# Kernel tuning notes

Hardware: AMD Instinct MI355X
Metric: run time of the kernel (lower is better)

The kernel has to match this reference:

```python
import jax, jax.numpy as jnp
import numpy as np

B, NF, IN = 8, 4096, 512
NB, NW, CD = 2, 320, 384  # num_codebooks, num_codewords, codeword_dim (d_model=NB*CD=768)
TAU = 1.0


def setup_inputs() -> dict:
    key = jax.random.key(0)
    k0, k1, k2, k3, k4 = jax.random.split(key, 5)
    x = jax.random.normal(k0, (B, NF, IN), dtype=jnp.float32)
    mask = jax.random.randint(k1, (B, NF), 0, 2) == 1  # True = invalid frame
    u = jax.random.uniform(k2, (B, NF, NB, NW), jnp.float32, 1e-6, 1.0 - 1e-6)
    gumbel = -jnp.log(-jnp.log(u))
    # projection Linear(IN -> NB*NW)
    W = jax.random.normal(k3, (IN, NB * NW), jnp.float32) * np.float32(1.0 / np.sqrt(IN))
    b = jnp.zeros((NB * NW,), jnp.float32)
    # codebooks, xavier-uniform-ish init
    limit = np.float32(np.sqrt(6.0 / (NW + CD)))
    codebooks = jax.random.uniform(k4, (NB, NW, CD), jnp.float32, -limit, limit)
    return dict(x=x, W=W, b=b, codebooks=codebooks, gumbel=gumbel, mask=mask)


def reference(x, W, b, codebooks, gumbel, mask):
    Bx, NFx = x.shape[:2]
    logits = (x @ W + b).reshape(Bx, NFx, NB, NW)  # (b, nf, nb, nw)
    # hard gumbel-softmax with straight-through estimator (training path)
    y = (logits + gumbel) / TAU
    soft = jax.nn.softmax(y, axis=-1)
    hard = jax.nn.one_hot(jnp.argmax(y, axis=-1), NW, dtype=soft.dtype)
    word_probs = hard + soft - jax.lax.stop_gradient(soft)
    # diversity perplexity from plain softmax probs, masked; note: faithful to
    # source, normalization divides by mask.sum() (count of invalid frames)
    soft_probs = jax.nn.softmax(logits, axis=-1)
    valid = (~mask)[..., None, None].astype(soft_probs.dtype)
    marginal = jnp.sum(soft_probs * valid, axis=(0, 1)) / mask.sum().astype(soft_probs.dtype)
    perplexity = jnp.exp(-jnp.sum(marginal * jnp.log(marginal + 1e-7), axis=-1)).sum()
    # quantize: one-hot gather-sum over codewords, concat codebooks -> d_model
    quantized = jnp.einsum('bfnw,nwd->bfnd', word_probs, codebooks).reshape(Bx, NFx, NB * CD)
    return quantized, perplexity
```

## Files before the change

kernel.cpp:

```cpp
#include <hip/hip_runtime.h>
#include <math.h>

#define BQ   8
#define NFQ  4096
#define INQ  512
#define NBQ  2
#define NWQ  320
#define CDQ  384
#define MQ   (BQ*NFQ)
#define NTOT (NBQ*NWQ)
#define DMOD (NBQ*CDQ)
#define QOUT ((size_t)MQ*(size_t)DMOD)

#define THREADS 512
#define BM 64
#define BK 32
#define NCH (INQ/BK)
#define NMB (MQ/BM)

#define A0B 0
#define A1B 4096
#define B0B 8192
#define B1B 28672
#define SMEMB 49152
#define SSUMB 8192
#define AYMB  9216
#define AIDXB 10240
#define SCB   11264
#define IDXB  11520
#define CALB  11776

#define WT_OFF   0
#define PART_OFF 655360
#define CS_OFF   1310720
#define MC_OFF   1313280

typedef __attribute__((ext_vector_type(4))) float f32x4;
typedef __attribute__((ext_vector_type(8))) short short8;
typedef const __attribute__((address_space(1))) unsigned short gas_us;
typedef __attribute__((address_space(3))) unsigned short las_us;

static __device__ __forceinline__ unsigned f2bf(float f) {
    unsigned u = __float_as_uint(f);
    return (u + 0x7FFFu + ((u >> 16) & 1u)) >> 16;
}

static __device__ __forceinline__ uint4 pack8u(float4 a, float4 b) {
    return make_uint4(f2bf(a.x) | (f2bf(a.y) << 16),
                      f2bf(a.z) | (f2bf(a.w) << 16),
                      f2bf(b.x) | (f2bf(b.y) << 16),
                      f2bf(b.z) | (f2bf(b.w) << 16));
}

#define MCOL(M,N) \
  acc##M##N = __builtin_amdgcn_mfma_f32_16x16x32_bf16(fa##M, fb##N, acc##M##N,0,0,0);

#define STAGE_B(KC, BASE) do { \
  const unsigned short* wp_ = WtB + (KC)*BK; \
  __builtin_amdgcn_global_load_lds((gas_us*)(wp_ + gb0), (las_us*)(smem + (BASE) + lo0), 16, 0, 0); \
  __builtin_amdgcn_global_load_lds((gas_us*)(wp_ + gb1), (las_us*)(smem + (BASE) + lo1), 16, 0, 0); \
  if (tid < 256) \
    __builtin_amdgcn_global_load_lds((gas_us*)(wp_ + gb2), (las_us*)(smem + (BASE) + lo2), 16, 0, 0); \
} while(0)

#define EPI1(M,R) do { \
  const int row_ = rh*32 + M*16 + q*4 + (R); \
  const int gm_  = m0 + row_; \
  float s_ = __expf(acc##M##0[R]) + __expf(acc##M##1[R]) + __expf(acc##M##2[R]) \
           + __expf(acc##M##3[R]) + __expf(acc##M##4[R]); \
  s_ += __shfl_xor(s_,1,64); s_ += __shfl_xor(s_,2,64); \
  s_ += __shfl_xor(s_,4,64); s_ += __shfl_xor(s_,8,64); \
  const float* gp_ = gum + (size_t)gm_*NTOT + nb*NWQ + cg*80 + c15; \
  float ym_ = acc##M##0[R] + gp_[0]; int yi_ = c15; float yt_; \
  yt_ = acc##M##1[R] + gp_[16]; if (yt_>ym_){ym_=yt_; yi_=16+c15;} \
  yt_ = acc##M##2[R] + gp_[32]; if (yt_>ym_){ym_=yt_; yi_=32+c15;} \
  yt_ = acc##M##3[R] + gp_[48]; if (yt_>ym_){ym_=yt_; yi_=48+c15;} \
  yt_ = acc##M##4[R] + gp_[64]; if (yt_>ym_){ym_=yt_; yi_=64+c15;} \
  yi_ += cg*80; \
  { float ov_; int oi_; \
    ov_=__shfl_xor(ym_,1,64); oi_=__shfl_xor(yi_,1,64); if(ov_>ym_||(ov_==ym_&&oi_<yi_)){ym_=ov_;yi_=oi_;} \
    ov_=__shfl_xor(ym_,2,64); oi_=__shfl_xor(yi_,2,64); if(ov_>ym_||(ov_==ym_&&oi_<yi_)){ym_=ov_;yi_=oi_;} \
    ov_=__shfl_xor(ym_,4,64); oi_=__shfl_xor(yi_,4,64); if(ov_>ym_||(ov_==ym_&&oi_<yi_)){ym_=ov_;yi_=oi_;} \
    ov_=__shfl_xor(ym_,8,64); oi_=__shfl_xor(yi_,8,64); if(ov_>ym_||(ov_==ym_&&oi_<yi_)){ym_=ov_;yi_=oi_;} } \
  if (c15 == 0) { \
    ((float*)(smem+SSUMB))[cg*64 + row_] = s_; \
    ((float*)(smem+AYMB ))[cg*64 + row_] = ym_; \
    ((int*  )(smem+AIDXB))[cg*64 + row_] = yi_; } \
} while(0)

#define EPI2(M,R) do { \
  const int row_ = rh*32 + M*16 + q*4 + (R); \
  const float sc_ = ((float*)(smem+SCB))[row_]; \
  ca0 = fmaf(__expf(acc##M##0[R]), sc_, ca0); \
  ca1 = fmaf(__expf(acc##M##1[R]), sc_, ca1); \
  ca2 = fmaf(__expf(acc##M##2[R]), sc_, ca2); \
  ca3 = fmaf(__expf(acc##M##3[R]), sc_, ca3); \
  ca4 = fmaf(__expf(acc##M##4[R]), sc_, ca4); \
} while(0)

__global__ __launch_bounds__(256) void wcvt(const float* __restrict__ W,
                                            unsigned short* __restrict__ Wt)
{
    __shared__ __align__(16) float sm[64][68];
    const int kb = blockIdx.x, cbk = blockIdx.y;
    const int tid = threadIdx.x;
    const int r = tid >> 2, qq = tid & 3;
    const float* wp = W + (size_t)(kb*64 + r)*NTOT + cbk*64;
    *(float4*)(&sm[r][(qq   )*4]) = *(const float4*)(wp + (qq   )*4);
    *(float4*)(&sm[r][(qq+ 4)*4]) = *(const float4*)(wp + (qq+ 4)*4);
    *(float4*)(&sm[r][(qq+ 8)*4]) = *(const float4*)(wp + (qq+ 8)*4);
    *(float4*)(&sm[r][(qq+12)*4]) = *(const float4*)(wp + (qq+12)*4);
    __syncthreads();
    const int cc = tid >> 2, kq = tid & 3;
    const int k0 = kq * 16;
    const float v0=sm[k0+0][cc],  v1=sm[k0+1][cc],  v2=sm[k0+2][cc],  v3=sm[k0+3][cc],
                v4=sm[k0+4][cc],  v5=sm[k0+5][cc],  v6=sm[k0+6][cc],  v7=sm[k0+7][cc],
                v8=sm[k0+8][cc],  v9=sm[k0+9][cc],  v10=sm[k0+10][cc],v11=sm[k0+11][cc],
                v12=sm[k0+12][cc],v13=sm[k0+13][cc],v14=sm[k0+14][cc],v15=sm[k0+15][cc];
    const unsigned u0 = f2bf(v0)  | (f2bf(v1) <<16), u1 = f2bf(v2)  | (f2bf(v3) <<16),
                   u2 = f2bf(v4)  | (f2bf(v5) <<16), u3 = f2bf(v6)  | (f2bf(v7) <<16),
                   u4 = f2bf(v8)  | (f2bf(v9) <<16), u5 = f2bf(v10) | (f2bf(v11)<<16),
                   u6 = f2bf(v12) | (f2bf(v13)<<16), u7 = f2bf(v14) | (f2bf(v15)<<16);
    unsigned short* op = Wt + (size_t)(cbk*64 + cc)*INQ + kb*64 + k0;
    *(uint4*)(op)     = make_uint4(u0,u1,u2,u3);
    *(uint4*)(op + 8) = make_uint4(u4,u5,u6,u7);
}

__global__ __launch_bounds__(THREADS, 4) void qk1(
    const float* __restrict__ x, const unsigned short* __restrict__ Wt,
    const float* __restrict__ bias, const float* __restrict__ cb,
    const float* __restrict__ gum, const int* __restrict__ maskp,
    float* __restrict__ out, unsigned short* __restrict__ partial)
{
    __shared__ __align__(16) char smem[SMEMB];
    const int tid = threadIdx.x;
    const int bid = blockIdx.x;
    const int mb = bid >> 1, nb = bid & 1;
    const int m0 = mb * BM;
    const int w = tid >> 6, l = tid & 63, q = l >> 4, c15 = l & 15;
    const int cg = w & 3, rh = w >> 2;

    const int sB = tid & 3;
    const int colj0 = (tid      ) >> 2, colj1 = (tid +  512) >> 2,
              colj2 = (tid + 1024) >> 2;
    const int kgj0 = sB ^ ((colj0 >> 1) & 3), kgj1 = sB ^ ((colj1 >> 1) & 3),
              kgj2 = sB ^ ((colj2 >> 1) & 3);
    const unsigned short* WtB = Wt + (size_t)nb * NWQ * INQ;
    const int gb0 = colj0*INQ + kgj0*8, gb1 = colj1*INQ + kgj1*8,
              gb2 = colj2*INQ + kgj2*8;
    const int lo0 = (tid      )*16, lo1 = (tid+ 512)*16, lo2 = (tid+1024)*16;

    const int xrow = tid >> 2, xh = tid & 3;
    const float* xg = x + (size_t)(m0 + xrow)*INQ + xh*8;
    const int axw = xrow*64 + ((xh ^ ((xrow >> 1) & 3)) * 16);

    const int sw = (c15 >> 1) & 3;
    const int aoff = (rh*32 + c15)*64 + ((q ^ sw) * 16);
    const int boff = (cg*80 + c15)*64 + ((q ^ sw) * 16);

    f32x4 acc00={0,0,0,0}, acc01={0,0,0,0}, acc02={0,0,0,0}, acc03={0,0,0,0}, acc04={0,0,0,0};
    f32x4 acc10={0,0,0,0}, acc11={0,0,0,0}, acc12={0,0,0,0}, acc13={0,0,0,0}, acc14={0,0,0,0};

    STAGE_B(0, B0B);
    if (tid < 256) {
        const float4 a0 = *(const float4*)(xg), a1 = *(const float4*)(xg + 4);
        *(uint4*)(smem + A0B + axw) = pack8u(a0, a1);
    }
    __syncthreads();

#pragma unroll 2
    for (int kc = 0; kc < NCH; ++kc) {
        const int p = kc & 1;
        const int Acur = p ? A1B : A0B;
        const int Anx  = p ? A0B : A1B;
        const int Bcur = p ? B1B : B0B;
        const int Bnx  = p ? B0B : B1B;
        const bool more = (kc + 1 < NCH);
        float4 n0, n1;
        if (more) {
            if (tid < 256) {
                n0 = *(const float4*)(xg + (kc+1)*BK);
                n1 = *(const float4*)(xg + (kc+1)*BK + 4);
            }
            STAGE_B(kc + 1, Bnx);
        }
        const short8 fa0 = *(const short8*)(smem + Acur + aoff);
        const short8 fa1 = *(const short8*)(smem + Acur + aoff + 1024);
        const short8 fb0 = *(const short8*)(smem + Bcur + boff);
        const short8 fb1 = *(const short8*)(smem + Bcur + boff + 1024);
        const short8 fb2 = *(const short8*)(smem + Bcur + boff + 2048);
        const short8 fb3 = *(const short8*)(smem + Bcur + boff + 3072);
        const short8 fb4 = *(const short8*)(smem + Bcur + boff + 4096);
        MCOL(0,0); MCOL(0,1); MCOL(0,2); MCOL(0,3); MCOL(0,4);
        MCOL(1,0); MCOL(1,1); MCOL(1,2); MCOL(1,3); MCOL(1,4);
        if (more && tid < 256)
            *(uint4*)(smem + Anx + axw) = pack8u(n0, n1);
        __syncthreads();
    }

    const float* bp = bias + nb*NWQ + cg*80 + c15;
    const float b0v = bp[0], b1v = bp[16], b2v = bp[32], b3v = bp[48], b4v = bp[64];
    acc00 = acc00 + b0v; acc01 = acc01 + b1v; acc02 = acc02 + b2v;
    acc03 = acc03 + b3v; acc04 = acc04 + b4v;
    acc10 = acc10 + b0v; acc11 = acc11 + b1v; acc12 = acc12 + b2v;
    acc13 = acc13 + b3v; acc14 = acc14 + b4v;

    EPI1(0,0); EPI1(0,1); EPI1(0,2); EPI1(0,3);
    EPI1(1,0); EPI1(1,1); EPI1(1,2); EPI1(1,3);
    __syncthreads();

    if (tid < BM) {
        const int row = tid;
        const float* ssum = (const float*)(smem + SSUMB);
        const float* aym  = (const float*)(smem + AYMB);
        const int*   aidx = (const int*)(smem + AIDXB);
        const float se = ssum[row] + ssum[64+row] + ssum[128+row] + ssum[192+row];
        const float vf = (maskp[m0 + row] == 0) ? 1.0f : 0.0f;
        ((float*)(smem + SCB))[row] = vf / se;
        float bv = aym[row]; int bi = aidx[row];
        float ov; int oi;
        ov = aym[ 64+row]; oi = aidx[ 64+row]; if (ov>bv || (ov==bv && oi<bi)) { bv=ov; bi=oi; }
        ov = aym[128+row]; oi = aidx[128+row]; if (ov>bv || (ov==bv && oi<bi)) { bv=ov; bi=oi; }
        ov = aym[192+row]; oi = aidx[192+row]; if (ov>bv || (ov==bv && oi<bi)) { bv=ov; bi=oi; }
        ((int*)(smem + IDXB))[row] = bi;
    }
    __syncthreads();

    float ca0=0.f, ca1=0.f, ca2=0.f, ca3=0.f, ca4=0.f;
    EPI2(0,0); EPI2(0,1); EPI2(0,2); EPI2(0,3);
    EPI2(1,0); EPI2(1,1); EPI2(1,2); EPI2(1,3);
    ca0 += __shfl_xor(ca0,16,64); ca0 += __shfl_xor(ca0,32,64);
    ca1 += __shfl_xor(ca1,16,64); ca1 += __shfl_xor(ca1,32,64);
    ca2 += __shfl_xor(ca2,16,64); ca2 += __shfl_xor(ca2,32,64);
    ca3 += __shfl_xor(ca3,16,64); ca3 += __shfl_xor(ca3,32,64);
    ca4 += __shfl_xor(ca4,16,64); ca4 += __shfl_xor(ca4,32,64);
    if (l < 16) {
        float* cal = (float*)(smem + CALB) + w*80 + c15;
        cal[0]=ca0; cal[16]=ca1; cal[32]=ca2; cal[48]=ca3; cal[64]=ca4;
    }
    __syncthreads();
    if (tid < NWQ) {
        const float* cal = (const float*)(smem + CALB);
        const float v = cal[tid] + cal[tid + 320];
        partial[(size_t)mb*NTOT + nb*NWQ + tid] = (unsigned short)f2bf(v);
    }

    const float* cbb = cb + (size_t)nb*NWQ*CDQ;
    const int* idxs = (const int*)(smem + IDXB);
    for (int t = tid; t < BM*(CDQ/4); t += THREADS) {
        const int r = t / (CDQ/4);
        const int qq = t - r*(CDQ/4);
        const int idx = idxs[r];
        float4 v = *(const float4*)(cbb + (size_t)idx*CDQ + qq*4);
        *(float4*)(out + (size_t)(m0+r)*DMOD + (size_t)nb*CDQ + qq*4) = v;
    }
}

__global__ __launch_bounds__(256) void qk2a(const unsigned short* __restrict__ partial,
                                            const int* __restrict__ maskp,
                                            float* __restrict__ colsum,
                                            int* __restrict__ maskcnt)
{
    __shared__ float fs[256];
    __shared__ int   is[4];
    const int b = blockIdx.x, tid = threadIdx.x;
    if (b < 40) {
        const int ci = tid & 15, g = tid >> 4;
        const int col = b*16 + ci;
        float s = 0.f;
        for (int r = 0; r < 32; ++r) {
            const unsigned u = partial[(size_t)(g*32 + r)*NTOT + col];
            s += __uint_as_float(u << 16);
        }
        fs[g*16 + ci] = s;
        __syncthreads();
        if (tid < 16) {
            float t = 0.f;
            for (int g2 = 0; g2 < 16; ++g2) t += fs[g2*16 + tid];
            colsum[b*16 + tid] = t;
        }
    } else {
        const int bb = b - 40;
        int ms = 0;
        for (int k2 = 0; k2 < 16; ++k2) ms += maskp[bb*4096 + tid + k2*256];
        for (int s2 = 32; s2 >= 1; s2 >>= 1) ms += __shfl_xor(ms, s2, 64);
        if ((tid & 63) == 0) is[tid >> 6] = ms;
        __syncthreads();
        if (tid == 0) maskcnt[bb] = is[0] + is[1] + is[2] + is[3];
    }
}

__global__ void qk2b(const float* __restrict__ colsum,
                     const int* __restrict__ maskcnt,
                     float* __restrict__ out)
{
    __shared__ float fred[10];
    __shared__ float s_ms;
    const int tid = threadIdx.x, lane = tid & 63, wid = tid >> 6;
    if (tid == 0) {
        int t = 0;
        for (int i = 0; i < 8; ++i) t += maskcnt[i];
        s_ms = (float)t;
    }
    __syncthreads();
    float mar = colsum[tid] / s_ms;
    float tv = mar * logf(mar + 1e-7f);
    for (int s = 32; s >= 1; s >>= 1) tv += __shfl_xor(tv, s, 64);
    if (lane == 0) fred[wid] = tv;
    __syncthreads();
    if (tid == 0) {
        float h0 = fred[0]+fred[1]+fred[2]+fred[3]+fred[4];
        float h1 = fred[5]+fred[6]+fred[7]+fred[8]+fred[9];
        out[QOUT] = expf(-h0) + expf(-h1);
    }
}

extern "C" void kernel_launch(void* const* d_in, const int* in_sizes, int n_in,
                              void* d_out, int out_size, void* d_ws, size_t ws_size,
                              hipStream_t stream) {
    const float* x    = (const float*)d_in[0];
    const float* W    = (const float*)d_in[1];
    const float* bias = (const float*)d_in[2];
    const float* cb   = (const float*)d_in[3];
    const float* gum  = (const float*)d_in[4];
    const int*   mask = (const int*)d_in[5];
    float* out = (float*)d_out;
    unsigned short* Wt      = (unsigned short*)((char*)d_ws + WT_OFF);
    unsigned short* partial = (unsigned short*)((char*)d_ws + PART_OFF);
    float*          colsum  = (float*)((char*)d_ws + CS_OFF);
    int*            maskcnt = (int*)((char*)d_ws + MC_OFF);

    wcvt<<<dim3(INQ/64, NTOT/64), 256, 0, stream>>>(W, Wt);
    qk1<<<NMB*NBQ, THREADS, 0, stream>>>(x, Wt, bias, cb, gum, mask, out, partial);
    qk2a<<<48, 256, 0, stream>>>(partial, mask, colsum, maskcnt);
    qk2b<<<1, 640, 0, stream>>>(colsum, maskcnt, out);
}
```

Before: 77.81 us.

## Warp-specialize GEMM main loop: B-loaders and A-converters with deeper x prefetch

Splits the 8 waves into two roles: waves 0-3 issue all the direct-to-LDS weight loads (five per thread instead of three spread across the block), and waves 4-7 load the fp32 x tile, convert it to bf16 and write it to LDS. The x register prefetch now runs two chunks ahead, and the main loop is manually unrolled with explicit waitcnt plus s_barrier instead of __syncthreads. The goal is to hide global load latency behind the MFMAs and to remove divergent per-thread guards. In exchange the work per wave is unbalanced and the explicit waitcnt(0) forces the loader waves to stall on their loads before each barrier.

```diff
diff --git a/kernel.cpp b/kernel.cpp
--- a/kernel.cpp
+++ b/kernel.cpp
@@ -59,8 +59,29 @@
   const unsigned short* wp_ = WtB + (KC)*BK; \
   __builtin_amdgcn_global_load_lds((gas_us*)(wp_ + gb0), (las_us*)(smem + (BASE) + lo0), 16, 0, 0); \
   __builtin_amdgcn_global_load_lds((gas_us*)(wp_ + gb1), (las_us*)(smem + (BASE) + lo1), 16, 0, 0); \
-  if (tid < 256) \
-    __builtin_amdgcn_global_load_lds((gas_us*)(wp_ + gb2), (las_us*)(smem + (BASE) + lo2), 16, 0, 0); \
+  __builtin_amdgcn_global_load_lds((gas_us*)(wp_ + gb2), (las_us*)(smem + (BASE) + lo2), 16, 0, 0); \
+  __builtin_amdgcn_global_load_lds((gas_us*)(wp_ + gb3), (las_us*)(smem + (BASE) + lo3), 16, 0, 0); \
+  __builtin_amdgcn_global_load_lds((gas_us*)(wp_ + gb4), (las_us*)(smem + (BASE) + lo4), 16, 0, 0); \
+} while(0)
+
+#define KBODY(KC, CUR0, CUR1, NXT0, NXT1, ACUR, ANXT, BCUR, BNXT) do { \
+  if (isB) { STAGE_B((KC)+1, BNXT); } \
+  else { NXT0 = *(const float4*)(xg + ((KC)+2)*BK); \
+         NXT1 = *(const float4*)(xg + ((KC)+2)*BK + 4); } \
+  const short8 fa0 = *(const short8*)(smem + (ACUR) + aoff); \
+  const short8 fa1 = *(const short8*)(smem + (ACUR) + aoff + 1024); \
+  const short8 fb0 = *(const short8*)(smem + (BCUR) + boff); \
+  const short8 fb1 = *(const short8*)(smem + (BCUR) + boff + 1024); \
+  const short8 fb2 = *(const short8*)(smem + (BCUR) + boff + 2048); \
+  const short8 fb3 = *(const short8*)(smem + (BCUR) + boff + 3072); \
+  const short8 fb4 = *(const short8*)(smem + (BCUR) + boff + 4096); \
+  MCOL(0,0); MCOL(0,1); MCOL(0,2); MCOL(0,3); MCOL(0,4); \
+  MCOL(1,0); MCOL(1,1); MCOL(1,2); MCOL(1,3); MCOL(1,4); \
+  if (isB) { asm volatile("s_waitcnt vmcnt(0)" ::: "memory"); } \
+  else     { *(uint4*)(smem + (ANXT) + axw) = pack8u(CUR0, CUR1); } \
+  asm volatile("s_waitcnt lgkmcnt(0)" ::: "memory"); \
+  __builtin_amdgcn_s_barrier(); \
+  asm volatile("" ::: "memory"); \
 } while(0)
 
 #define EPI1(M,R) do { \
@@ -139,18 +160,24 @@
     const int m0 = mb * BM;
     const int w = tid >> 6, l = tid & 63, q = l >> 4, c15 = l & 15;
     const int cg = w & 3, rh = w >> 2;
+    const bool isB = (w < 4);
 
     const int sB = tid & 3;
-    const int colj0 = (tid      ) >> 2, colj1 = (tid +  512) >> 2,
-              colj2 = (tid + 1024) >> 2;
+    const int colj0 = (tid      ) >> 2, colj1 = (tid +  256) >> 2,
+              colj2 = (tid + 512) >> 2, colj3 = (tid +  768) >> 2,
+              colj4 = (tid +1024) >> 2;
     const int kgj0 = sB ^ ((colj0 >> 1) & 3), kgj1 = sB ^ ((colj1 >> 1) & 3),
-              kgj2 = sB ^ ((colj2 >> 1) & 3);
+              kgj2 = sB ^ ((colj2 >> 1) & 3), kgj3 = sB ^ ((colj3 >> 1) & 3),
+              kgj4 = sB ^ ((colj4 >> 1) & 3);
     const unsigned short* WtB = Wt + (size_t)nb * NWQ * INQ;
     const int gb0 = colj0*INQ + kgj0*8, gb1 = colj1*INQ + kgj1*8,
-              gb2 = colj2*INQ + kgj2*8;
-    const int lo0 = (tid      )*16, lo1 = (tid+ 512)*16, lo2 = (tid+1024)*16;
-
-    const int xrow = tid >> 2, xh = tid & 3;
+              gb2 = colj2*INQ + kgj2*8, gb3 = colj3*INQ + kgj3*8,
+              gb4 = colj4*INQ + kgj4*8;
+    const int lo0 = (tid      )*16, lo1 = (tid+ 256)*16, lo2 = (tid+ 512)*16,
+              lo3 = (tid+ 768)*16, lo4 = (tid+1024)*16;
+
+    const int xt = tid & 255;
+    const int xrow = xt >> 2, xh = xt & 3;
     const float* xg = x + (size_t)(m0 + xrow)*INQ + xh*8;
     const int axw = xrow*64 + ((xh ^ ((xrow >> 1) & 3)) * 16);
 
@@ -160,42 +187,52 @@
 
     f32x4 acc00={0,0,0,0}, acc01={0,0,0,0}, acc02={0,0,0,0}, acc03={0,0,0,0}, acc04={0,0,0,0};
     f32x4 acc10={0,0,0,0}, acc11={0,0,0,0}, acc12={0,0,0,0}, acc13={0,0,0,0}, acc14={0,0,0,0};
-
-    STAGE_B(0, B0B);
-    if (tid < 256) {
+    float4 mv0, mv1, nv0, nv1;
+
+    if (isB) {
+        STAGE_B(0, B0B);
+        asm volatile("s_waitcnt vmcnt(0)" ::: "memory");
+    } else {
         const float4 a0 = *(const float4*)(xg), a1 = *(const float4*)(xg + 4);
         *(uint4*)(smem + A0B + axw) = pack8u(a0, a1);
-    }
-    __syncthreads();
-
-#pragma unroll 2
-    for (int kc = 0; kc < NCH; ++kc) {
-        const int p = kc & 1;
-        const int Acur = p ? A1B : A0B;
-        const int Anx  = p ? A0B : A1B;
-        const int Bcur = p ? B1B : B0B;
-        const int Bnx  = p ? B0B : B1B;
-        const bool more = (kc + 1 < NCH);
-        float4 n0, n1;
-        if (more) {
-            if (tid < 256) {
-                n0 = *(const float4*)(xg + (kc+1)*BK);
-                n1 = *(const float4*)(xg + (kc+1)*BK + 4);
-            }
-            STAGE_B(kc + 1, Bnx);
-        }
-        const short8 fa0 = *(const short8*)(smem + Acur + aoff);
-        const short8 fa1 = *(const short8*)(smem + Acur + aoff + 1024);
-        const short8 fb0 = *(const short8*)(smem + Bcur + boff);
-        const short8 fb1 = *(const short8*)(smem + Bcur + boff + 1024);
-        const short8 fb2 = *(const short8*)(smem + Bcur + boff + 2048);
-        const short8 fb3 = *(const short8*)(smem + Bcur + boff + 3072);
-        const short8 fb4 = *(const short8*)(smem + Bcur + boff + 4096);
+        mv0 = *(const float4*)(xg + BK);
+        mv1 = *(const float4*)(xg + BK + 4);
+    }
+    asm volatile("s_waitcnt lgkmcnt(0)" ::: "memory");
+    __builtin_amdgcn_s_barrier();
+    asm volatile("" ::: "memory");
+
+    for (int kc2 = 0; kc2 < 14; kc2 += 2) {
+        KBODY(kc2,   mv0, mv1, nv0, nv1, A0B, A1B, B0B, B1B);
+        KBODY(kc2+1, nv0, nv1, mv0, mv1, A1B, A0B, B1B, B0B);
+    }
+    {
+        if (isB) STAGE_B(15, B1B);
+        const short8 fa0 = *(const short8*)(smem + A0B + aoff);
+        const short8 fa1 = *(const short8*)(smem + A0B + aoff + 1024);
+        const short8 fb0 = *(const short8*)(smem + B0B + boff);
+        const short8 fb1 = *(const short8*)(smem + B0B + boff + 1024);
+        const short8 fb2 = *(const short8*)(smem + B0B + boff + 2048);
+        const short8 fb3 = *(const short8*)(smem + B0B + boff + 3072);
+        const short8 fb4 = *(const short8*)(smem + B0B + boff + 4096);
         MCOL(0,0); MCOL(0,1); MCOL(0,2); MCOL(0,3); MCOL(0,4);
         MCOL(1,0); MCOL(1,1); MCOL(1,2); MCOL(1,3); MCOL(1,4);
-        if (more && tid < 256)
-            *(uint4*)(smem + Anx + axw) = pack8u(n0, n1);
-        __syncthreads();
+        if (isB) { asm volatile("s_waitcnt vmcnt(0)" ::: "memory"); }
+        else     { *(uint4*)(smem + A1B + axw) = pack8u(mv0, mv1); }
+        asm volatile("s_waitcnt lgkmcnt(0)" ::: "memory");
+        __builtin_amdgcn_s_barrier();
+        asm volatile("" ::: "memory");
+    }
+    {
+        const short8 fa0 = *(const short8*)(smem + A1B + aoff);
+        const short8 fa1 = *(const short8*)(smem + A1B + aoff + 1024);
+        const short8 fb0 = *(const short8*)(smem + B1B + boff);
+        const short8 fb1 = *(const short8*)(smem + B1B + boff + 1024);
+        const short8 fb2 = *(const short8*)(smem + B1B + boff + 2048);
+        const short8 fb3 = *(const short8*)(smem + B1B + boff + 3072);
+        const short8 fb4 = *(const short8*)(smem + B1B + boff + 4096);
+        MCOL(0,0); MCOL(0,1); MCOL(0,2); MCOL(0,3); MCOL(0,4);
+        MCOL(1,0); MCOL(1,1); MCOL(1,2); MCOL(1,3); MCOL(1,4);
     }
 
     const float* bp = bias + nb*NWQ + cg*80 + c15;
```

After: 79.32 us. No clear change (+1.9%).

## Double fused GEMM row tile to 128 for more B-tile reuse

Applied to the files above, without the earlier changes.

Raises the M tile of the fused projection/argmax/softmax kernel from 64 to 128 rows, so each wave computes four 16-row MFMA passes instead of two. Each staged W tile is now reused across twice as many rows, and all 512 threads load the A tile instead of half. The epilogue scratch buffers are re-laid out and the partial-sum reduction kernel is adjusted for half as many row blocks. The cost is 20 accumulator vectors per thread instead of 10, which raises register pressure and may lower occupancy, and the grid has half as many blocks.

```diff
diff --git a/kernel.cpp b/kernel.cpp
--- a/kernel.cpp
+++ b/kernel.cpp
@@ -13,22 +13,22 @@
 #define QOUT ((size_t)MQ*(size_t)DMOD)
 
 #define THREADS 512
-#define BM 64
+#define BM 128
 #define BK 32
 #define NCH (INQ/BK)
 #define NMB (MQ/BM)
 
 #define A0B 0
-#define A1B 4096
-#define B0B 8192
-#define B1B 28672
-#define SMEMB 49152
-#define SSUMB 8192
-#define AYMB  9216
-#define AIDXB 10240
-#define SCB   11264
-#define IDXB  11520
-#define CALB  11776
+#define A1B 8192
+#define B0B 16384
+#define B1B 36864
+#define SMEMB 57344
+#define SSUMB 0
+#define AYMB  2048
+#define AIDXB 4096
+#define SCB   6144
+#define IDXB  6656
+#define CALB  16384
 
 #define WT_OFF   0
 #define PART_OFF 655360
@@ -54,6 +54,11 @@
 
 #define MCOL(M,N) \
   acc##M##N = __builtin_amdgcn_mfma_f32_16x16x32_bf16(fa##M, fb##N, acc##M##N,0,0,0);
+
+#define MPASS(M, ABASE) do { \
+  const short8 fa##M = *(const short8*)(smem + (ABASE) + aoff + (M)*1024); \
+  MCOL(M,0); MCOL(M,1); MCOL(M,2); MCOL(M,3); MCOL(M,4); \
+} while(0)
 
 #define STAGE_B(KC, BASE) do { \
   const unsigned short* wp_ = WtB + (KC)*BK; \
@@ -64,7 +69,7 @@
 } while(0)
 
 #define EPI1(M,R) do { \
-  const int row_ = rh*32 + M*16 + q*4 + (R); \
+  const int row_ = rh*64 + (M)*16 + q*4 + (R); \
   const int gm_  = m0 + row_; \
   float s_ = __expf(acc##M##0[R]) + __expf(acc##M##1[R]) + __expf(acc##M##2[R]) \
            + __expf(acc##M##3[R]) + __expf(acc##M##4[R]); \
@@ -83,13 +88,13 @@
     ov_=__shfl_xor(ym_,4,64); oi_=__shfl_xor(yi_,4,64); if(ov_>ym_||(ov_==ym_&&oi_<yi_)){ym_=ov_;yi_=oi_;} \
     ov_=__shfl_xor(ym_,8,64); oi_=__shfl_xor(yi_,8,64); if(ov_>ym_||(ov_==ym_&&oi_<yi_)){ym_=ov_;yi_=oi_;} } \
   if (c15 == 0) { \
-    ((float*)(smem+SSUMB))[cg*64 + row_] = s_; \
-    ((float*)(smem+AYMB ))[cg*64 + row_] = ym_; \
-    ((int*  )(smem+AIDXB))[cg*64 + row_] = yi_; } \
+    ((float*)(smem+SSUMB))[cg*128 + row_] = s_; \
+    ((float*)(smem+AYMB ))[cg*128 + row_] = ym_; \
+    ((int*  )(smem+AIDXB))[cg*128 + row_] = yi_; } \
 } while(0)
 
 #define EPI2(M,R) do { \
-  const int row_ = rh*32 + M*16 + q*4 + (R); \
+  const int row_ = rh*64 + (M)*16 + q*4 + (R); \
   const float sc_ = ((float*)(smem+SCB))[row_]; \
   ca0 = fmaf(__expf(acc##M##0[R]), sc_, ca0); \
   ca1 = fmaf(__expf(acc##M##1[R]), sc_, ca1); \
@@ -155,14 +160,16 @@
     const int axw = xrow*64 + ((xh ^ ((xrow >> 1) & 3)) * 16);
 
     const int sw = (c15 >> 1) & 3;
-    const int aoff = (rh*32 + c15)*64 + ((q ^ sw) * 16);
+    const int aoff = (rh*64 + c15)*64 + ((q ^ sw) * 16);
     const int boff = (cg*80 + c15)*64 + ((q ^ sw) * 16);
 
     f32x4 acc00={0,0,0,0}, acc01={0,0,0,0}, acc02={0,0,0,0}, acc03={0,0,0,0}, acc04={0,0,0,0};
     f32x4 acc10={0,0,0,0}, acc11={0,0,0,0}, acc12={0,0,0,0}, acc13={0,0,0,0}, acc14={0,0,0,0};
+    f32x4 acc20={0,0,0,0}, acc21={0,0,0,0}, acc22={0,0,0,0}, acc23={0,0,0,0}, acc24={0,0,0,0};
+    f32x4 acc30={0,0,0,0}, acc31={0,0,0,0}, acc32={0,0,0,0}, acc33={0,0,0,0}, acc34={0,0,0,0};
 
     STAGE_B(0, B0B);
-    if (tid < 256) {
+    {
         const float4 a0 = *(const float4*)(xg), a1 = *(const float4*)(xg + 4);
         *(uint4*)(smem + A0B + axw) = pack8u(a0, a1);
     }
@@ -178,35 +185,32 @@
         const bool more = (kc + 1 < NCH);
         float4 n0, n1;
         if (more) {
-            if (tid < 256) {
-                n0 = *(const float4*)(xg + (kc+1)*BK);
-                n1 = *(const float4*)(xg + (kc+1)*BK + 4);
-            }
+            n0 = *(const float4*)(xg + (kc+1)*BK);
+            n1 = *(const float4*)(xg + (kc+1)*BK + 4);
             STAGE_B(kc + 1, Bnx);
         }
-        const short8 fa0 = *(const short8*)(smem + Acur + aoff);
-        const short8 fa1 = *(const short8*)(smem + Acur + aoff + 1024);
         const short8 fb0 = *(const short8*)(smem + Bcur + boff);
         const short8 fb1 = *(const short8*)(smem + Bcur + boff + 1024);
         const short8 fb2 = *(const short8*)(smem + Bcur + boff + 2048);
         const short8 fb3 = *(const short8*)(smem + Bcur + boff + 3072);
         const short8 fb4 = *(const short8*)(smem + Bcur + boff + 4096);
-        MCOL(0,0); MCOL(0,1); MCOL(0,2); MCOL(0,3); MCOL(0,4);
-        MCOL(1,0); MCOL(1,1); MCOL(1,2); MCOL(1,3); MCOL(1,4);
-        if (more && tid < 256)
+        MPASS(0, Acur); MPASS(1, Acur); MPASS(2, Acur); MPASS(3, Acur);
+        if (more)
             *(uint4*)(smem + Anx + axw) = pack8u(n0, n1);
         __syncthreads();
     }
 
     const float* bp = bias + nb*NWQ + cg*80 + c15;
     const float b0v = bp[0], b1v = bp[16], b2v = bp[32], b3v = bp[48], b4v = bp[64];
-    acc00 = acc00 + b0v; acc01 = acc01 + b1v; acc02 = acc02 + b2v;
-    acc03 = acc03 + b3v; acc04 = acc04 + b4v;
-    acc10 = acc10 + b0v; acc11 = acc11 + b1v; acc12 = acc12 + b2v;
-    acc13 = acc13 + b3v; acc14 = acc14 + b4v;
+    acc00 = acc00 + b0v; acc01 = acc01 + b1v; acc02 = acc02 + b2v; acc03 = acc03 + b3v; acc04 = acc04 + b4v;
+    acc10 = acc10 + b0v; acc11 = acc11 + b1v; acc12 = acc12 + b2v; acc13 = acc13 + b3v; acc14 = acc14 + b4v;
+    acc20 = acc20 + b0v; acc21 = acc21 + b1v; acc22 = acc22 + b2v; acc23 = acc23 + b3v; acc24 = acc24 + b4v;
+    acc30 = acc30 + b0v; acc31 = acc31 + b1v; acc32 = acc32 + b2v; acc33 = acc33 + b3v; acc34 = acc34 + b4v;
 
     EPI1(0,0); EPI1(0,1); EPI1(0,2); EPI1(0,3);
     EPI1(1,0); EPI1(1,1); EPI1(1,2); EPI1(1,3);
+    EPI1(2,0); EPI1(2,1); EPI1(2,2); EPI1(2,3);
+    EPI1(3,0); EPI1(3,1); EPI1(3,2); EPI1(3,3);
     __syncthreads();
 
     if (tid < BM) {
@@ -214,14 +218,14 @@
         const float* ssum = (const float*)(smem + SSUMB);
         const float* aym  = (const float*)(smem + AYMB);
         const int*   aidx = (const int*)(smem + AIDXB);
-        const float se = ssum[row] + ssum[64+row] + ssum[128+row] + ssum[192+row];
+        const float se = ssum[row] + ssum[128+row] + ssum[256+row] + ssum[384+row];
         const float vf = (maskp[m0 + row] == 0) ? 1.0f : 0.0f;
         ((float*)(smem + SCB))[row] = vf / se;
         float bv = aym[row]; int bi = aidx[row];
         float ov; int oi;
-        ov = aym[ 64+row]; oi = aidx[ 64+row]; if (ov>bv || (ov==bv && oi<bi)) { bv=ov; bi=oi; }
         ov = aym[128+row]; oi = aidx[128+row]; if (ov>bv || (ov==bv && oi<bi)) { bv=ov; bi=oi; }
-        ov = aym[192+row]; oi = aidx[192+row]; if (ov>bv || (ov==bv && oi<bi)) { bv=ov; bi=oi; }
+        ov = aym[256+row]; oi = aidx[256+row]; if (ov>bv || (ov==bv && oi<bi)) { bv=ov; bi=oi; }
+        ov = aym[384+row]; oi = aidx[384+row]; if (ov>bv || (ov==bv && oi<bi)) { bv=ov; bi=oi; }
         ((int*)(smem + IDXB))[row] = bi;
     }
     __syncthreads();
@@ -229,6 +233,8 @@
     float ca0=0.f, ca1=0.f, ca2=0.f, ca3=0.f, ca4=0.f;
     EPI2(0,0); EPI2(0,1); EPI2(0,2); EPI2(0,3);
     EPI2(1,0); EPI2(1,1); EPI2(1,2); EPI2(1,3);
+    EPI2(2,0); EPI2(2,1); EPI2(2,2); EPI2(2,3);
+    EPI2(3,0); EPI2(3,1); EPI2(3,2); EPI2(3,3);
     ca0 += __shfl_xor(ca0,16,64); ca0 += __shfl_xor(ca0,32,64);
     ca1 += __shfl_xor(ca1,16,64); ca1 += __shfl_xor(ca1,32,64);
     ca2 += __shfl_xor(ca2,16,64); ca2 += __shfl_xor(ca2,32,64);
@@ -268,8 +274,8 @@
         const int ci = tid & 15, g = tid >> 4;
         const int col = b*16 + ci;
         float s = 0.f;
-        for (int r = 0; r < 32; ++r) {
-            const unsigned u = partial[(size_t)(g*32 + r)*NTOT + col];
+        for (int r = 0; r < 16; ++r) {
+            const unsigned u = partial[(size_t)(g*16 + r)*NTOT + col];
             s += __uint_as_float(u << 16);
         }
         fs[g*16 + ci] = s;
```

Measured after the change: 82.50 us. 1.06x slower.
